# Kernel tuning notes

Hardware: AMD Instinct MI355X
Metric: run time of the kernel (lower is better)

The kernel has to match this reference:

```python
import jax, jax.numpy as jnp
import numpy as np

B, T, D, H = 2, 2048, 1024, 16
DH = D // H  # 64


def setup_inputs() -> dict:
    key = jax.random.key(0)
    ks = jax.random.split(key, 8)
    s = 0.02  # typical init scale for projection weights
    return {
        "query_states": jax.random.normal(ks[0], (B, T, D), jnp.float32),
        "key_states": jax.random.normal(ks[1], (B, T, D), jnp.float32),
        "attention_mask": jnp.zeros((B, 1, 1, T), jnp.float32),
        "Wq": jax.random.normal(ks[2], (D, D), jnp.float32) * s,
        "bq": jnp.zeros((D,), jnp.float32),
        "Wk": jax.random.normal(ks[3], (D, D), jnp.float32) * s,
        "bk": jnp.zeros((D,), jnp.float32),
        "Wv": jax.random.normal(ks[4], (D, D), jnp.float32) * s,
        "bv": jnp.zeros((D,), jnp.float32),
        "mask_future": 0,
    }


def _heads(x):
    # [B, T, D] -> [B, H, T, DH]
    b, t, _ = x.shape
    return x.reshape(b, t, H, DH).transpose(0, 2, 1, 3)


def reference(query_states, key_states, attention_mask, Wq, bq, Wk, bk, Wv, bv, mask_future):
    q = _heads(query_states @ Wq + bq)   # [B,H,T,DH]
    k = _heads(key_states @ Wk + bk)     # [B,H,T,DH]
    v = _heads(key_states @ Wv + bv)     # [B,H,T,DH]
    scale = 1.0 / jnp.sqrt(jnp.asarray(DH, jnp.float32))
    scores = jnp.einsum("bhqd,bhkd->bhqk", q, k) * scale + attention_mask
    if mask_future:  # static Python int flag
        t = scores.shape[-1]
        triu = jnp.triu(jnp.ones((t, t), bool))  # includes diagonal, as in torch.triu
        scores = jnp.where(triu, -jnp.inf, scores)
    probs = jax.nn.softmax(scores, axis=-1)
    # dropout p=0.0 -> identity
    ctx = jnp.einsum("bhqk,bhkd->bhqd", probs, v)  # [B,H,T,DH]
    b, _, t, _ = ctx.shape
    return ctx.transpose(0, 2, 1, 3).reshape(b, t, H * DH)
```

## Files before the change

kernel.cpp:

```cpp
#include <hip/hip_runtime.h>

#define DEV __device__ __forceinline__

typedef _Float16 f16;
typedef __attribute__((ext_vector_type(2))) _Float16 f16x2;
typedef __attribute__((ext_vector_type(4))) _Float16 f16x4;
typedef __attribute__((ext_vector_type(8))) _Float16 f16x8;
typedef __attribute__((ext_vector_type(4))) float f32x4;
typedef __attribute__((ext_vector_type(16))) float f32x16;
typedef __attribute__((ext_vector_type(4))) int i32x4;

constexpr int B = 2, T = 2048, D = 1024, H = 16, DH = 64;
constexpr int M = B * T;
constexpr float LOG2E = 1.4426950408889634f;

DEV void gload_lds16(const void* g, void* l) {
  __builtin_amdgcn_global_load_lds(
      (const __attribute__((address_space(1))) void*)g,
      (__attribute__((address_space(3))) void*)l, 16, 0, 0);
}

DEV unsigned pack_pk(float a, float b) {
  auto v = __builtin_amdgcn_cvt_pkrtz(a, b);
  return __builtin_bit_cast(unsigned, v);
}

DEV float redmax32(float x) { return fmaxf(x, __shfl_xor(x, 32, 64)); }
DEV float redsum32(float x) { return x + __shfl_xor(x, 32, 64); }

__global__ __launch_bounds__(256) void cast_f32_f16(
    const float* __restrict__ in, f16* __restrict__ out, int n) {
  int i = (blockIdx.x * 256 + threadIdx.x) * 8;
  if (i >= n) return;
  f32x4 a = *(const f32x4*)(in + i);
  f32x4 b = *(const f32x4*)(in + i + 4);
  f16x8 o;
  o[0] = (f16)a[0]; o[1] = (f16)a[1]; o[2] = (f16)a[2]; o[3] = (f16)a[3];
  o[4] = (f16)b[0]; o[5] = (f16)b[1]; o[6] = (f16)b[2]; o[7] = (f16)b[3];
  *(f16x8*)(out + i) = o;
}

__global__ __launch_bounds__(256) void transpose_cast(
    const float* __restrict__ Wq, const float* __restrict__ Wk,
    const float* __restrict__ Wv, f16* __restrict__ WT) {
  int mat = blockIdx.z;
  const float* W = (mat == 0) ? Wq : (mat == 1 ? Wk : Wv);
  f16* out = WT + (size_t)mat * D * D;
  __shared__ float tile[32][33];
  int nt = blockIdx.x * 32, kt = blockIdx.y * 32;
  int tx = threadIdx.x, ty = threadIdx.y;
  for (int j = 0; j < 4; ++j) {
    int r = ty + 8 * j;
    tile[r][tx] = W[(size_t)(kt + r) * D + nt + tx];
  }
  __syncthreads();
  for (int j = 0; j < 4; ++j) {
    int r = ty + 8 * j;
    out[(size_t)(nt + r) * D + kt + tx] = (f16)tile[tx][r];
  }
}

__global__ __launch_bounds__(256) void qkv_gemm(
    const f16* __restrict__ XQ, const f16* __restrict__ XK,
    const f16* __restrict__ WT, const float* __restrict__ bq,
    const float* __restrict__ bk, const float* __restrict__ bv,
    f16* __restrict__ QKV) {
  int mat = blockIdx.z;
  const f16* X = (mat == 0) ? XQ : XK;
  const f16* Wt = WT + (size_t)mat * D * D;
  const float* bias = (mat == 0) ? bq : (mat == 1 ? bk : bv);
  f16* out = QKV + (size_t)mat * M * D;
  float oscale = (mat == 0) ? 0.125f * LOG2E : 1.0f;
  int Lb = blockIdx.x + 8 * blockIdx.y;
  int n0 = (Lb & 7) * 128, m0 = (Lb >> 3) * 128;

  __shared__ f16 lA[128 * 64];
  __shared__ f16 lB[128 * 64];
  char* lAb = (char*)lA;
  char* lBb = (char*)lB;

  int tid = threadIdx.x;
  int w = tid >> 6, lane = tid & 63;
  int l15 = lane & 15, lhi = lane >> 4;
  int wr = w >> 1, wc = w & 1;
  int r8 = lane >> 3, slot = lane & 7;
  int sslot = slot ^ r8;

  f32x4 acc[4][4] = {};

  for (int kt = 0; kt < D / 64; ++kt) {
    __syncthreads();
    for (int i = 0; i < 4; ++i) {
      int chunk = w * 4 + i;
      int row = chunk * 8 + r8;
      const f16* srcA = X + (size_t)(m0 + row) * D + kt * 64 + sslot * 8;
      gload_lds16(srcA, lAb + chunk * 1024);
      const f16* srcB = Wt + (size_t)(n0 + row) * D + kt * 64 + sslot * 8;
      gload_lds16(srcB, lBb + chunk * 1024);
    }
    __syncthreads();
    for (int ks = 0; ks < 2; ++ks) {
      f16x8 aF[4], bF[4];
      for (int mt = 0; mt < 4; ++mt) {
        int row = wr * 64 + mt * 16 + l15;
        int byt = (row * 128 + ks * 64 + lhi * 16) ^ ((row & 7) << 4);
        aF[mt] = *(const f16x8*)(lAb + byt);
      }
      for (int nt = 0; nt < 4; ++nt) {
        int row = wc * 64 + nt * 16 + l15;
        int byt = (row * 128 + ks * 64 + lhi * 16) ^ ((row & 7) << 4);
        bF[nt] = *(const f16x8*)(lBb + byt);
      }
      for (int mt = 0; mt < 4; ++mt)
        for (int nt = 0; nt < 4; ++nt)
          acc[mt][nt] = __builtin_amdgcn_mfma_f32_16x16x32_f16(
              aF[mt], bF[nt], acc[mt][nt], 0, 0, 0);
    }
  }

  float bv4[4];
  for (int nt = 0; nt < 4; ++nt) bv4[nt] = bias[n0 + wc * 64 + nt * 16 + l15];
  if (mat < 2) {
    for (int mt = 0; mt < 4; ++mt)
      for (int nt = 0; nt < 4; ++nt) {
        int col = n0 + wc * 64 + nt * 16 + l15;
        int hh = col >> 6, dh = col & 63;
        for (int r = 0; r < 4; ++r) {
          int row = m0 + wr * 64 + mt * 16 + lhi * 4 + r;
          int bb = row >> 11, tt = row & (T - 1);
          out[((size_t)(bb * H + hh) * T + tt) * 64 + dh] =
              (f16)((acc[mt][nt][r] + bv4[nt]) * oscale);
        }
      }
  } else {
    for (int mt = 0; mt < 4; ++mt)
      for (int nt = 0; nt < 4; ++nt) {
        int col = n0 + wc * 64 + nt * 16 + l15;
        int hh = col >> 6, dh = col & 63;
        int row0 = m0 + wr * 64 + mt * 16 + lhi * 4;
        int bb = row0 >> 11, tt = row0 & (T - 1);
        f16x4 pk;
        for (int r = 0; r < 4; ++r) pk[r] = (f16)(acc[mt][nt][r] + bv4[nt]);
        *(f16x4*)(out + ((size_t)(bb * H + hh) * 64 + dh) * T + tt) = pk;
      }
  }
}

__global__ __launch_bounds__(256) void attn(
    const f16* __restrict__ QKV, const float* __restrict__ mask,
    const int* __restrict__ mfp, float* __restrict__ out) {
  int L = blockIdx.x + 16 * blockIdx.y + 256 * blockIdx.z;
  int e = L & 7, q = L >> 3;
  int bh = e * 4 + (q & 3);
  int q0 = (q >> 2) * 128;
  int b = bh >> 4, h = bh & 15;
  int mf = *mfp;
  constexpr int NT = T / 64;

  const f16* Qh = QKV + (size_t)bh * T * 64;
  const f16* Kh = QKV + (size_t)M * D + (size_t)bh * T * 64;
  const f16* VTh = QKV + (size_t)2 * M * D + (size_t)bh * 64 * T;

  __shared__ f16 sK[2][64 * 64];
  __shared__ f16 sVT[2][64 * 64];

  int tid = threadIdx.x;
  int w = tid >> 6, lane = tid & 63;
  int l31 = lane & 31, hi = lane >> 5;
  int qrow = q0 + w * 32 + l31;

  const float* mb = mask + (size_t)b * T;
  bool lnz = false;
#pragma unroll
  for (int j = 0; j < 8; ++j) {
    f32x4 mv = *(const f32x4*)(mb + lane * 32 + j * 4);
    lnz |= (mv[0] != 0.f) | (mv[1] != 0.f) | (mv[2] != 0.f) | (mv[3] != 0.f);
  }
  int domask = __any(lnz) | mf;

  f16x8 qF[4];
  const f16* qp = Qh + (size_t)qrow * 64;
#pragma unroll
  for (int kc = 0; kc < 4; ++kc) qF[kc] = *(const f16x8*)(qp + kc * 16 + hi * 8);

  auto STAGE = [&](int kv0, int buf) {
    char* dK = (char*)sK[buf];
    char* dV = (char*)sVT[buf];
#pragma unroll
    for (int i = 0; i < 2; ++i) {
      int c = (w * 2 + i) * 64 + lane;
      int r = c >> 3;
      int slot = (c & 7) ^ (r & 7);
      gload_lds16(Kh + (size_t)(kv0 + r) * 64 + slot * 8, dK + (w * 2 + i) * 1024);
      gload_lds16(VTh + (size_t)r * T + kv0 + slot * 8, dV + (w * 2 + i) * 1024);
    }
  };

  float mprev = -1e30f, lsum = 0.f;
  f32x16 oAcc[2] = {};
  STAGE(0, 0);
  __syncthreads();

  for (int t = 0; t < NT; ++t) {
    if (t) __syncthreads();
    if (t + 1 < NT) STAGE((t + 1) * 64, (t + 1) & 1);
    int kv0 = t * 64;
    const char* bK = (const char*)sK[t & 1];
    const char* bV = (const char*)sVT[t & 1];

    f32x16 sA[2] = {};
#pragma unroll
    for (int f = 0; f < 2; ++f)
#pragma unroll
      for (int kc = 0; kc < 4; ++kc) {
        int row = f * 32 + l31;
        f16x8 kF = *(const f16x8*)(bK + ((row * 128 + kc * 32 + hi * 16) ^ ((row & 7) << 4)));
        sA[f] = __builtin_amdgcn_mfma_f32_32x32x16_f16(kF, qF[kc], sA[f], 0, 0, 0);
      }

    float mx = -1e30f;
    if (domask) {
#pragma unroll
      for (int f = 0; f < 2; ++f)
#pragma unroll
        for (int r = 0; r < 16; ++r) {
          int kv = kv0 + f * 32 + (r & 3) + 8 * (r >> 2) + 4 * hi;
          float v = sA[f][r] + LOG2E * mb[kv];
          if (mf && kv >= qrow) v = -1e30f;
          sA[f][r] = v;
          mx = fmaxf(mx, v);
        }
    } else {
#pragma unroll
      for (int f = 0; f < 2; ++f)
#pragma unroll
        for (int r = 0; r < 16; ++r) mx = fmaxf(mx, sA[f][r]);
    }
    mx = redmax32(mx);

    if (!__all(mx <= mprev + 8.f)) {
      float mn = fmaxf(mprev, mx);
      float asc = __builtin_amdgcn_exp2f(mprev - mn);
      lsum *= asc;
#pragma unroll
      for (int f = 0; f < 2; ++f)
#pragma unroll
        for (int r = 0; r < 16; ++r) oAcc[f][r] *= asc;
      mprev = mn;
    }

    float rs = 0.f;
#pragma unroll
    for (int f = 0; f < 2; ++f)
#pragma unroll
      for (int r = 0; r < 16; ++r) {
        float e2 = __builtin_amdgcn_exp2f(sA[f][r] - mprev);
        sA[f][r] = e2;
        rs += e2;
      }
    lsum += redsum32(rs);

    f16x8 pF[4];
#pragma unroll
    for (int f = 0; f < 2; ++f) {
      unsigned pk_[8], px_[8];
#pragma unroll
      for (int g = 0; g < 8; ++g) {
        pk_[g] = pack_pk(sA[f][2 * g], sA[f][2 * g + 1]);
        px_[g] = (unsigned)__shfl_xor((int)pk_[g], 32, 64);
      }
#pragma unroll
      for (int half = 0; half < 2; ++half) {
        int o = half * 4;
        i32x4 d;
        d[0] = (int)(hi ? px_[o + 2] : pk_[o + 0]);
        d[1] = (int)(hi ? px_[o + 3] : pk_[o + 1]);
        d[2] = (int)(hi ? pk_[o + 2] : px_[o + 0]);
        d[3] = (int)(hi ? pk_[o + 3] : px_[o + 1]);
        pF[f * 2 + half] = __builtin_bit_cast(f16x8, d);
      }
    }

#pragma unroll
    for (int df = 0; df < 2; ++df)
#pragma unroll
      for (int kc = 0; kc < 4; ++kc) {
        int row = df * 32 + l31;
        f16x8 vF = *(const f16x8*)(bV + ((row * 128 + kc * 32 + hi * 16) ^ ((row & 7) << 4)));
        oAcc[df] = __builtin_amdgcn_mfma_f32_32x32x16_f16(vF, pF[kc], oAcc[df], 0, 0, 0);
      }
  }

  float linv = 1.0f / lsum;
  float* op = out + (size_t)(b * T + qrow) * D + h * 64;
#pragma unroll
  for (int df = 0; df < 2; ++df)
#pragma unroll
    for (int g = 0; g < 4; ++g) {
      f32x4 ov;
#pragma unroll
      for (int r2 = 0; r2 < 4; ++r2) ov[r2] = oAcc[df][g * 4 + r2] * linv;
      *(f32x4*)(op + df * 32 + g * 8 + hi * 4) = ov;
    }
}

extern "C" void kernel_launch(void* const* d_in, const int* in_sizes, int n_in,
                              void* d_out, int out_size, void* d_ws, size_t ws_size,
                              hipStream_t stream) {
  const float* q_in = (const float*)d_in[0];
  const float* k_in = (const float*)d_in[1];
  const float* amask = (const float*)d_in[2];
  const float* Wq = (const float*)d_in[3];
  const float* bq = (const float*)d_in[4];
  const float* Wk = (const float*)d_in[5];
  const float* bk = (const float*)d_in[6];
  const float* Wv = (const float*)d_in[7];
  const float* bv = (const float*)d_in[8];
  const int* mf = (const int*)d_in[9];
  float* out = (float*)d_out;

  char* ws = (char*)d_ws;
  f16* XQ = (f16*)ws;
  f16* XK = (f16*)(ws + (((size_t)8) << 20));
  f16* WT = (f16*)(ws + (((size_t)16) << 20));
  f16* QKV = (f16*)(ws + (((size_t)24) << 20));

  cast_f32_f16<<<2048, 256, 0, stream>>>(q_in, XQ, M * D);
  cast_f32_f16<<<2048, 256, 0, stream>>>(k_in, XK, M * D);
  transpose_cast<<<dim3(32, 32, 3), dim3(32, 8), 0, stream>>>(Wq, Wk, Wv, WT);
  qkv_gemm<<<dim3(8, 32, 3), 256, 0, stream>>>(XQ, XK, WT, bq, bk, bv, QKV);
  attn<<<dim3(16, 16, 2), 256, 0, stream>>>(QKV, amask, mf, out);
}
```

Measured before the change: 218.5 us.

## Use permlane32 swaps, MFMA priority hints, max3 reductions and LDS-staged output stores

Result: no change. 214.9 us (-1.7%).

```diff
diff --git a/kernel.cpp b/kernel.cpp
--- a/kernel.cpp
+++ b/kernel.cpp
@@ -25,8 +25,30 @@
   return __builtin_bit_cast(unsigned, v);
 }
 
+DEV float max3f(float a, float b, float c) { return fmaxf(fmaxf(a, b), c); }
+
+#if __has_builtin(__builtin_amdgcn_permlane32_swap)
+#define HAVE_PLSWAP 1
+DEV void swap32(unsigned& a, unsigned& b) {
+  auto r = __builtin_amdgcn_permlane32_swap((int)a, (int)b, false, false);
+  a = (unsigned)r[0];
+  b = (unsigned)r[1];
+}
+DEV float redmax32(float x) {
+  unsigned a = __builtin_bit_cast(unsigned, x), b = a;
+  swap32(a, b);
+  return fmaxf(__builtin_bit_cast(float, a), __builtin_bit_cast(float, b));
+}
+DEV float redsum32(float x) {
+  unsigned a = __builtin_bit_cast(unsigned, x), b = a;
+  swap32(a, b);
+  return __builtin_bit_cast(float, a) + __builtin_bit_cast(float, b);
+}
+#else
+#define HAVE_PLSWAP 0
 DEV float redmax32(float x) { return fmaxf(x, __shfl_xor(x, 32, 64)); }
 DEV float redsum32(float x) { return x + __shfl_xor(x, 32, 64); }
+#endif
 
 __global__ __launch_bounds__(256) void cast_f32_f16(
     const float* __restrict__ in, f16* __restrict__ out, int n) {
@@ -161,8 +183,7 @@
   const f16* Kh = QKV + (size_t)M * D + (size_t)bh * T * 64;
   const f16* VTh = QKV + (size_t)2 * M * D + (size_t)bh * 64 * T;
 
-  __shared__ f16 sK[2][64 * 64];
-  __shared__ f16 sVT[2][64 * 64];
+  __shared__ char smem[32768];
 
   int tid = threadIdx.x;
   int w = tid >> 6, lane = tid & 63;
@@ -184,8 +205,8 @@
   for (int kc = 0; kc < 4; ++kc) qF[kc] = *(const f16x8*)(qp + kc * 16 + hi * 8);
 
   auto STAGE = [&](int kv0, int buf) {
-    char* dK = (char*)sK[buf];
-    char* dV = (char*)sVT[buf];
+    char* dK = smem + buf * 8192;
+    char* dV = smem + 16384 + buf * 8192;
 #pragma unroll
     for (int i = 0; i < 2; ++i) {
       int c = (w * 2 + i) * 64 + lane;
@@ -205,10 +226,11 @@
     if (t) __syncthreads();
     if (t + 1 < NT) STAGE((t + 1) * 64, (t + 1) & 1);
     int kv0 = t * 64;
-    const char* bK = (const char*)sK[t & 1];
-    const char* bV = (const char*)sVT[t & 1];
+    const char* bK = smem + (t & 1) * 8192;
+    const char* bV = smem + 16384 + (t & 1) * 8192;
 
     f32x16 sA[2] = {};
+    __builtin_amdgcn_s_setprio(1);
 #pragma unroll
     for (int f = 0; f < 2; ++f)
 #pragma unroll
@@ -217,9 +239,11 @@
         f16x8 kF = *(const f16x8*)(bK + ((row * 128 + kc * 32 + hi * 16) ^ ((row & 7) << 4)));
         sA[f] = __builtin_amdgcn_mfma_f32_32x32x16_f16(kF, qF[kc], sA[f], 0, 0, 0);
       }
-
-    float mx = -1e30f;
+    __builtin_amdgcn_s_setprio(0);
+
+    float mx;
     if (domask) {
+      mx = -1e30f;
 #pragma unroll
       for (int f = 0; f < 2; ++f)
 #pragma unroll
@@ -231,10 +255,21 @@
           mx = fmaxf(mx, v);
         }
     } else {
-#pragma unroll
-      for (int f = 0; f < 2; ++f)
-#pragma unroll
-        for (int r = 0; r < 16; ++r) mx = fmaxf(mx, sA[f][r]);
+      float t0 = max3f(sA[0][0], sA[0][1], sA[0][2]);
+      float t1 = max3f(sA[0][3], sA[0][4], sA[0][5]);
+      float t2 = max3f(sA[0][6], sA[0][7], sA[0][8]);
+      float t3 = max3f(sA[0][9], sA[0][10], sA[0][11]);
+      float t4 = max3f(sA[0][12], sA[0][13], sA[0][14]);
+      float t5 = max3f(sA[1][0], sA[1][1], sA[1][2]);
+      float t6 = max3f(sA[1][3], sA[1][4], sA[1][5]);
+      float t7 = max3f(sA[1][6], sA[1][7], sA[1][8]);
+      float t8 = max3f(sA[1][9], sA[1][10], sA[1][11]);
+      float t9 = max3f(sA[1][12], sA[1][13], sA[1][14]);
+      float u0 = max3f(t0, t1, t2);
+      float u1 = max3f(t3, t4, sA[0][15]);
+      float u2 = max3f(t5, t6, t7);
+      float u3 = max3f(t8, t9, sA[1][15]);
+      mx = fmaxf(max3f(u0, u1, u2), u3);
     }
     mx = redmax32(mx);
 
@@ -261,6 +296,22 @@
     lsum += redsum32(rs);
 
     f16x8 pF[4];
+#if HAVE_PLSWAP
+#pragma unroll
+    for (int f = 0; f < 2; ++f)
+#pragma unroll
+      for (int half = 0; half < 2; ++half) {
+        unsigned p0 = pack_pk(sA[f][half * 8 + 0], sA[f][half * 8 + 1]);
+        unsigned p1 = pack_pk(sA[f][half * 8 + 2], sA[f][half * 8 + 3]);
+        unsigned p2 = pack_pk(sA[f][half * 8 + 4], sA[f][half * 8 + 5]);
+        unsigned p3 = pack_pk(sA[f][half * 8 + 6], sA[f][half * 8 + 7]);
+        swap32(p0, p2);
+        swap32(p1, p3);
+        i32x4 d;
+        d[0] = (int)p0; d[1] = (int)p1; d[2] = (int)p2; d[3] = (int)p3;
+        pF[f * 2 + half] = __builtin_bit_cast(f16x8, d);
+      }
+#else
 #pragma unroll
     for (int f = 0; f < 2; ++f) {
       unsigned pk_[8], px_[8];
@@ -280,7 +331,9 @@
         pF[f * 2 + half] = __builtin_bit_cast(f16x8, d);
       }
     }
-
+#endif
+
+    __builtin_amdgcn_s_setprio(1);
 #pragma unroll
     for (int df = 0; df < 2; ++df)
 #pragma unroll
@@ -289,19 +342,26 @@
         f16x8 vF = *(const f16x8*)(bV + ((row * 128 + kc * 32 + hi * 16) ^ ((row & 7) << 4)));
         oAcc[df] = __builtin_amdgcn_mfma_f32_32x32x16_f16(vF, pF[kc], oAcc[df], 0, 0, 0);
       }
-  }
-
+    __builtin_amdgcn_s_setprio(0);
+  }
+
+  __syncthreads();
   float linv = 1.0f / lsum;
-  float* op = out + (size_t)(b * T + qrow) * D + h * 64;
+  float* sOw = (float*)smem + w * 2048;
 #pragma unroll
   for (int df = 0; df < 2; ++df)
 #pragma unroll
-    for (int g = 0; g < 4; ++g) {
-      f32x4 ov;
-#pragma unroll
-      for (int r2 = 0; r2 < 4; ++r2) ov[r2] = oAcc[df][g * 4 + r2] * linv;
-      *(f32x4*)(op + df * 32 + g * 8 + hi * 4) = ov;
-    }
+    for (int r = 0; r < 16; ++r) {
+      int d = df * 32 + 4 * hi + (r & 3) + 8 * (r >> 2);
+      sOw[l31 * 64 + (d ^ l31)] = oAcc[df][r] * linv;
+    }
+  __syncthreads();
+  float* op0 = out + (size_t)(b * T + q0 + w * 32) * D + h * 64;
+#pragma unroll
+  for (int r2 = 0; r2 < 32; ++r2) {
+    float v = sOw[r2 * 64 + (lane ^ r2)];
+    op0[(size_t)r2 * D + lane] = v;
+  }
 }
 
 extern "C" void kernel_launch(void* const* d_in, const int* in_sizes, int n_in,
```
